# Kernel tuning notes

Measured on AMD Instinct MI355X. Metric: run time of the kernel, lower is better.

## Reference

```python
import jax, jax.numpy as jnp
import numpy as np

N_EMBD = 1024
N_HEAD = 16
HEAD_DIM = N_EMBD // N_HEAD


def setup_inputs() -> dict:
    key = jax.random.key(0)
    ks = jax.random.split(key, 5)
    B, T = 4, 2048
    s = 0.02
    return {
        "x": jax.random.normal(ks[0], (B, T, N_EMBD), dtype=jnp.float32),
        "w_qkv": jax.random.normal(ks[1], (N_EMBD, 3 * N_EMBD), dtype=jnp.float32) * s,
        "b_qkv": jnp.zeros((3 * N_EMBD,), dtype=jnp.float32),
        "w_out": jax.random.normal(ks[2], (N_EMBD, N_EMBD), dtype=jnp.float32) * s,
        "b_out": jnp.zeros((N_EMBD,), dtype=jnp.float32),
    }


def reference(x, w_qkv, b_qkv, w_out, b_out):
    # Eval-mode forward (dropout disabled), matching the torch module's math.
    B, T, C = x.shape
    qkv = x @ w_qkv + b_qkv                      # [B,T,3C]
    q, k, v = jnp.split(qkv, 3, axis=-1)
    def heads(t):
        return t.reshape(B, T, N_HEAD, HEAD_DIM).transpose(0, 2, 1, 3)  # [B,H,T,D]
    q, k, v = heads(q), heads(k), heads(v)
    scores = jnp.einsum("bhtd,bhsd->bhts", q, k) / jnp.sqrt(jnp.float32(HEAD_DIM))
    causal = jnp.tril(jnp.ones((T, T), dtype=bool))
    scores = jnp.where(causal[None, None], scores, -jnp.inf)
    attn = jax.nn.softmax(scores, axis=-1)       # [B,H,T,T]
    y = jnp.einsum("bhts,bhsd->bhtd", attn, v)   # [B,H,T,D]
    y = y.transpose(0, 2, 1, 3).reshape(B, T, C)
    return y @ w_out + b_out
```

## Files before the change

### kernel.cpp

```cpp
#include <hip/hip_runtime.h>
#include <hip/hip_bf16.h>

#define TSEQ 2048
#define CEMB 1024

typedef __attribute__((ext_vector_type(8))) short bf16x8;
typedef __attribute__((ext_vector_type(4))) float f32x4;
typedef __attribute__((ext_vector_type(16))) float f32x16;
typedef __attribute__((ext_vector_type(4))) int i32x4;

__device__ __forceinline__ unsigned short f2bf(float f){
  return __builtin_bit_cast(unsigned short, __float2bfloat16(f));
}

__device__ __forceinline__ f32x4 MFMA16(bf16x8 a, bf16x8 b, f32x4 c){
  return __builtin_amdgcn_mfma_f32_16x16x32_bf16(a, b, c, 0, 0, 0);
}

#define GLDS(src, dst) __builtin_amdgcn_global_load_lds( \
      (const __attribute__((address_space(1))) void*)(src), \
      (__attribute__((address_space(3))) void*)(dst), 16, 0, 0)

template<int N> __device__ __forceinline__ void vmwait(){
  if constexpr (N == 0) asm volatile("s_waitcnt vmcnt(0)" ::: "memory");
  else if constexpr (N == 6) asm volatile("s_waitcnt vmcnt(6)" ::: "memory");
  else if constexpr (N == 7) asm volatile("s_waitcnt vmcnt(7)" ::: "memory");
  else asm volatile("s_waitcnt vmcnt(8)" ::: "memory");
}

__global__ void k_cvt_bf16(const float* __restrict__ in, unsigned short* __restrict__ out, int n4){
  int i = blockIdx.x * blockDim.x + threadIdx.x;
  if (i >= n4) return;
  const float4 v = reinterpret_cast<const float4*>(in)[i];
  ushort4 o;
  o.x = f2bf(v.x); o.y = f2bf(v.y); o.z = f2bf(v.z); o.w = f2bf(v.w);
  reinterpret_cast<ushort4*>(out)[i] = o;
}

__global__ void k_transpose_bf16(const float* __restrict__ w, unsigned short* __restrict__ wT, int K, int N){
  __shared__ unsigned short tile[32][33];
  const int n0 = blockIdx.x * 32, k0 = blockIdx.y * 32;
  const int tx = threadIdx.x & 31, ty = threadIdx.x >> 5;
  #pragma unroll
  for (int r = 0; r < 4; ++r){
    int k = ty * 4 + r;
    tile[k][tx] = f2bf(w[(size_t)(k0 + k) * N + n0 + tx]);
  }
  __syncthreads();
  #pragma unroll
  for (int r = 0; r < 4; ++r){
    int n = ty * 4 + r;
    wT[(size_t)(n0 + n) * K + k0 + tx] = tile[tx][n];
  }
}

__global__ __launch_bounds__(256) void k_vT(const unsigned short* __restrict__ qkv,
                                            unsigned short* __restrict__ vT){
  __shared__ __align__(16) unsigned short tile[64*64];
  const int tid = threadIdx.x;
  const int bh = blockIdx.x;
  const int t0 = blockIdx.y * 64;
  const int b = bh >> 4, h = bh & 15;
  const int lt = tid >> 3, seg = tid & 7;
  #pragma unroll
  for (int r = 0; r < 2; ++r){
    const int t = lt + 32*r;
    const i32x4 v = *(const i32x4*)&qkv[((size_t)(b*TSEQ + t0 + t))*3072 + 2048 + h*64 + seg*8];
    const int slot = seg ^ (t & 7) ^ (t >> 3);
    *(i32x4*)((char*)tile + t*128 + slot*16) = v;
  }
  __syncthreads();
  const int w = tid >> 6, lane = tid & 63;
  const int tseg = lane & 7;
  #pragma unroll
  for (int r = 0; r < 2; ++r){
    const int d = w*8 + (lane>>3) + 32*r;
    unsigned int wd[4];
    #pragma unroll
    for (int jp = 0; jp < 4; ++jp){
      unsigned int lo, hi;
      #pragma unroll
      for (int e = 0; e < 2; ++e){
        const int j = jp*2 + e;
        const int t = tseg*8 + j;
        const int byteoff = t*128 + ((2*d) ^ (((j ^ tseg) & 7) << 4));
        const unsigned int val = *(const unsigned short*)((const char*)tile + byteoff);
        if (e == 0) lo = val; else hi = val;
      }
      wd[jp] = lo | (hi << 16);
    }
    i32x4 o4; o4[0]=wd[0]; o4[1]=wd[1]; o4[2]=wd[2]; o4[3]=wd[3];
    *(i32x4*)&vT[((size_t)bh*64 + d)*2048 + t0 + tseg*8] = o4;
  }
}

template<bool OUT_BF16, int BN>
__global__ __launch_bounds__(512, 2) void k_gemm256(
    const unsigned short* __restrict__ A,
    const unsigned short* __restrict__ Bt,
    const float* __restrict__ bias,
    void* __restrict__ Cout, int M, int N, int K)
{
  constexpr int NW  = BN / 64;
  constexpr int NH0 = (NW + 1) / 2;
  constexpr int NL  = 4 + NW;
  constexpr int BNB = BN * 128;
  __shared__ __align__(16) char smem[65536 + 2 * BNB];

  const int tid = threadIdx.x;
  const int lane = tid & 63, w = tid >> 6;
  const int wm = w >> 2, wn = w & 3;
  const int l15 = lane & 15, l4 = lane >> 4;
  const int x7 = l15 & 7;

  unsigned lin = blockIdx.x;
  {
    const unsigned nwg = gridDim.x;
    const unsigned qq = nwg >> 3, rr = nwg & 7;
    const unsigned xcd = lin & 7, loc = lin >> 3;
    lin = (xcd < rr ? xcd * (qq + 1) : rr * (qq + 1) + (xcd - rr) * qq) + loc;
  }
  const unsigned ntn = (unsigned)N / BN;
  const int m0 = (int)(lin / ntn) << 8;
  const int n0 = (int)(lin % ntn) * BN;

  const int srow = lane >> 3;
  const int scx  = (lane & 7) ^ srow;
  const unsigned short* Ag = A  + (size_t)(m0 + w*8 + srow) * K + scx * 8;
  const unsigned short* Bg = Bt + (size_t)(n0 + w*8 + srow) * K + scx * 8;

  auto stageA = [&](int buf, int kt){
    const unsigned short* s = Ag + kt*64;
    char* d = smem + buf*32768 + (w << 10);
    #pragma unroll
    for (int i = 0; i < 4; ++i) GLDS(s + (size_t)(i*64)*K, d + i*8192);
  };
  auto stageB = [&](int buf, int kt){
    const unsigned short* s = Bg + kt*64;
    char* d = smem + 65536 + buf*BNB + (w << 10);
    #pragma unroll
    for (int i = 0; i < NW; ++i) GLDS(s + (size_t)(i*64)*K, d + i*8192);
  };

  const int arow = wm*128 + l15;
  const int brow = wn*(BN/4) + l15;
  auto rdA = [&](int buf, int m, int ks)->bf16x8 {
    return *(const bf16x8*)(smem + buf*32768 + (arow + m*16)*128 + (((ks*4 + l4) ^ x7) << 4));
  };
  auto rdB = [&](int buf, int n, int ks)->bf16x8 {
    return *(const bf16x8*)(smem + 65536 + buf*BNB + (brow + n*16)*128 + (((ks*4 + l4) ^ x7) << 4));
  };

  f32x4 acc[8][NW] = {};
  const int NIT = K >> 7;

  stageA(0, 0); stageB(0, 0);
  stageA(1, 1); stageB(1, 1);
  vmwait<NL>();
  __builtin_amdgcn_s_barrier();
  asm volatile("" ::: "memory");

  for (int it = 0; it < NIT; ++it){
    const bool more = (it + 1 < NIT);
    #pragma unroll
    for (int half = 0; half < 2; ++half){
      const int buf = half;
      bf16x8 bfr[NW][2], af1[4][2], af2[4][2];
      #pragma unroll
      for (int n = 0; n < NW; ++n){ bfr[n][0] = rdB(buf, n, 0); bfr[n][1] = rdB(buf, n, 1); }
      #pragma unroll
      for (int m = 0; m < 4; ++m){ af1[m][0] = rdA(buf, m, 0); af1[m][1] = rdA(buf, m, 1); }
      __builtin_amdgcn_s_setprio(1);
      #pragma unroll
      for (int m = 0; m < 4; ++m)
        #pragma unroll
        for (int n = 0; n < NH0; ++n)
          #pragma unroll
          for (int ks = 0; ks < 2; ++ks)
            acc[m][n] = MFMA16(af1[m][ks], bfr[n][ks], acc[m][n]);
      __builtin_amdgcn_s_setprio(0);
      #pragma unroll
      for (int m = 0; m < 4; ++m){ af2[m][0] = rdA(buf, m+4, 0); af2[m][1] = rdA(buf, m+4, 1); }
      __builtin_amdgcn_s_setprio(1);
      #pragma unroll
      for (int m = 0; m < 4; ++m)
        #pragma unroll
        for (int n = NH0; n < NW; ++n)
          #pragma unroll
          for (int ks = 0; ks < 2; ++ks)
            acc[m][n] = MFMA16(af1[m][ks], bfr[n][ks], acc[m][n]);
      __builtin_amdgcn_s_setprio(0);
      __builtin_amdgcn_s_setprio(1);
      #pragma unroll
      for (int m = 0; m < 4; ++m)
        #pragma unroll
        for (int n = NH0; n < NW; ++n)
          #pragma unroll
          for (int ks = 0; ks < 2; ++ks)
            acc[m+4][n] = MFMA16(af2[m][ks], bfr[n][ks], acc[m+4][n]);
      __builtin_amdgcn_s_setprio(0);
      asm volatile("s_waitcnt lgkmcnt(0)" ::: "memory");
      __builtin_amdgcn_s_barrier();
      asm volatile("" ::: "memory");
      if (more){ stageA(buf, 2*it + half + 2); stageB(buf, 2*it + half + 2); }
      __builtin_amdgcn_s_setprio(1);
      #pragma unroll
      for (int m = 0; m < 4; ++m)
        #pragma unroll
        for (int n = 0; n < NH0; ++n)
          #pragma unroll
          for (int ks = 0; ks < 2; ++ks)
            acc[m+4][n] = MFMA16(af2[m][ks], bfr[n][ks], acc[m+4][n]);
      __builtin_amdgcn_s_setprio(0);
      if (more) vmwait<NL>();
      else      vmwait<0>();
      __builtin_amdgcn_s_barrier();
      asm volatile("" ::: "memory");
    }
  }

  float bv[NW];
  #pragma unroll
  for (int n = 0; n < NW; ++n) bv[n] = bias[n0 + wn*(BN/4) + n*16 + l15];

  #pragma unroll
  for (int m = 0; m < 8; ++m){
    const int row = m0 + wm*128 + m*16 + l4*4;
    #pragma unroll
    for (int n = 0; n < NW; ++n){
      const int col = n0 + wn*(BN/4) + n*16 + l15;
      #pragma unroll
      for (int r = 0; r < 4; ++r){
        float v = acc[m][n][r] + bv[n];
        if (OUT_BF16)
          ((unsigned short*)Cout)[(size_t)(row + r) * N + col] = f2bf(v);
        else
          ((float*)Cout)[(size_t)(row + r) * N + col] = v;
      }
    }
  }
}

__global__ __launch_bounds__(512, 4) void k_attn(
    const unsigned short* __restrict__ qkv,
    const unsigned short* __restrict__ vT,
    unsigned short* __restrict__ y)
{
  __shared__ __align__(16) char Ksm[2][8192];
  __shared__ __align__(16) char Vsm[2][8192];
  __shared__ float Ls[8][32];

  const int tid = threadIdx.x, lane = tid & 63, w = tid >> 6;
  const int q31 = lane & 31, hi = lane >> 5;
  const int bh = blockIdx.x, p = blockIdx.y;
  const int g = w >> 2, wl = w & 3;
  const int myt = g ? (15 - p) : p;
  const int b = bh >> 4, h = bh & 15;
  const size_t rowB = (size_t)b * TSEQ;

  const int wq0 = myt*128 + 32*wl, qg = wq0 + q31;
  const int nkt_my = 2*myt + 2;
  const int nktB  = 2*(15 - p) + 2;

  const float sc = 0.18033688011112042f;

  bf16x8 qf[4];
  {
    const unsigned short* qp = qkv + (rowB + qg) * 3072 + h * 64;
    #pragma unroll
    for (int c4 = 0; c4 < 4; ++c4){
      bf16x8 v = *(const bf16x8*)(qp + c4*16 + hi*8);
      #pragma unroll
      for (int j = 0; j < 8; ++j){
        const unsigned int bits = ((unsigned int)(unsigned short)v[j]) << 16;
        v[j] = (short)f2bf(__builtin_bit_cast(float, bits) * sc);
      }
      qf[c4] = v;
    }
  }

  const int kr = lane >> 3, sl = lane & 7, cx = sl ^ kr;
  const unsigned short* kgbase = qkv + (rowB + w*8 + kr) * 3072 + 1024 + h*64 + cx*8;
  const unsigned short* vgbase = vT + ((size_t)bh*64 + w*8 + kr) * 2048 + cx*8;

  #define STAGE(ktile, buf)                                                          \
    do {                                                                             \
      GLDS(kgbase + (size_t)(ktile)*64*3072, &Ksm[buf][0] + w*1024);                 \
      GLDS(vgbase + (ktile)*64,              &Vsm[buf][0] + w*1024);                 \
    } while (0)

  f32x16 O[2] = {};
  float l = 0.f;

  STAGE(0, 0);
  __syncthreads();

  int cbuf = 0;
  for (int kt = 0; kt < nktB; ++kt){
    if (kt + 1 < nktB) STAGE(kt + 1, cbuf ^ 1);

    if (kt < nkt_my){
      const char* kb = Ksm[cbuf];
      const char* vb = Vsm[cbuf];
      const bool domask = (kt*64 + 63 > wq0);
      #pragma unroll
      for (int sub = 0; sub < 2; ++sub){
        f32x16 S = {};
        __builtin_amdgcn_s_setprio(1);
        #pragma unroll
        for (int c4 = 0; c4 < 4; ++c4){
          const bf16x8 kf = *(const bf16x8*)(kb + (sub*32 + q31)*128
                                + ((((c4<<1)|hi) ^ (q31 & 7)) << 4));
          S = __builtin_amdgcn_mfma_f32_32x32x16_bf16(kf, qf[c4], S, 0, 0, 0);
        }
        __builtin_amdgcn_s_setprio(0);
        if (domask){
          #pragma unroll
          for (int r = 0; r < 16; ++r){
            const int kg = kt*64 + sub*32 + (r&3) + 8*(r>>2) + 4*hi;
            if (kg > qg) S[r] = -1e30f;
          }
        }
        float ps = 0.f;
        #pragma unroll
        for (int r = 0; r < 16; ++r){
          S[r] = __builtin_amdgcn_exp2f(S[r]);
          ps += S[r];
        }
        l += ps;
        bf16x8 paf[2];
        #pragma unroll
        for (int kc = 0; kc < 2; ++kc){
          const int e = kc * 8;
          unsigned int a, bb, cc, dd;
          asm("v_cvt_pk_bf16_f32 %0, %1, %2" : "=v"(a)  : "v"(S[e+0]), "v"(S[e+1]));
          asm("v_cvt_pk_bf16_f32 %0, %1, %2" : "=v"(bb) : "v"(S[e+4]), "v"(S[e+5]));
          asm("v_cvt_pk_bf16_f32 %0, %1, %2" : "=v"(cc) : "v"(S[e+2]), "v"(S[e+3]));
          asm("v_cvt_pk_bf16_f32 %0, %1, %2" : "=v"(dd) : "v"(S[e+6]), "v"(S[e+7]));
          asm volatile("v_permlane32_swap_b32 %0, %1" : "+v"(a),  "+v"(bb));
          asm volatile("v_permlane32_swap_b32 %0, %1" : "+v"(cc), "+v"(dd));
          i32x4 pwv; pwv[0] = (int)a; pwv[1] = (int)cc; pwv[2] = (int)bb; pwv[3] = (int)dd;
          paf[kc] = __builtin_bit_cast(bf16x8, pwv);
        }
        __builtin_amdgcn_s_setprio(1);
        #pragma unroll
        for (int kc = 0; kc < 2; ++kc){
          #pragma unroll
          for (int dblk = 0; dblk < 2; ++dblk){
            const int dr = dblk*32 + q31;
            const bf16x8 vf = *(const bf16x8*)(vb + dr*128
                                  + ((((sub<<2)|(kc<<1)|hi) ^ (dr & 7)) << 4));
            O[dblk] = __builtin_amdgcn_mfma_f32_32x32x16_bf16(paf[kc], vf, O[dblk], 0, 0, 0);
          }
        }
        __builtin_amdgcn_s_setprio(0);
      }
    }

    __syncthreads();
    cbuf ^= 1;
  }

  {
    const float lc = l + __shfl_xor(l, 32);
    if (lane < 32) Ls[w][lane] = 1.0f / lc;
  }
  __syncthreads();

  #pragma unroll
  for (int r = 0; r < 16; ++r){
    const int qloc = (r&3) + 8*(r>>2) + 4*hi;
    const float inv = Ls[w][qloc];
    const size_t row = rowB + wq0 + qloc;
    #pragma unroll
    for (int dblk = 0; dblk < 2; ++dblk)
      y[row * CEMB + h*64 + dblk*32 + q31] = f2bf(O[dblk][r] * inv);
  }
  #undef STAGE
}

extern "C" void kernel_launch(void* const* d_in, const int* in_sizes, int n_in,
                              void* d_out, int out_size, void* d_ws, size_t ws_size,
                              hipStream_t stream)
{
  const float* x     = (const float*)d_in[0];
  const float* w_qkv = (const float*)d_in[1];
  const float* b_qkv = (const float*)d_in[2];
  const float* w_out = (const float*)d_in[3];
  const float* b_out = (const float*)d_in[4];
  float* out = (float*)d_out;

  char* ws = (char*)d_ws;
  unsigned short* xb    = (unsigned short*)(ws);
  unsigned short* vTb   = (unsigned short*)(ws);
  unsigned short* qkvb  = (unsigned short*)(ws + (16u<<20));
  unsigned short* yb    = (unsigned short*)(ws + (64u<<20));
  unsigned short* wqkvT = (unsigned short*)(ws + (80u<<20));
  unsigned short* woutT = (unsigned short*)(ws + (86u<<20));

  const int M = 4 * TSEQ;

  k_cvt_bf16<<<(M * CEMB / 4 + 255) / 256, 256, 0, stream>>>(x, xb, M * CEMB / 4);
  k_transpose_bf16<<<dim3(3072/32, 1024/32), 256, 0, stream>>>(w_qkv, wqkvT, 1024, 3072);
  k_transpose_bf16<<<dim3(1024/32, 1024/32), 256, 0, stream>>>(w_out, woutT, 1024, 1024);

  k_gemm256<true, 192><<<dim3((M/256) * (3072/192)), 512, 0, stream>>>(xb, wqkvT, b_qkv, qkvb, M, 3072, 1024);
  k_vT<<<dim3(64, TSEQ/64), 256, 0, stream>>>(qkvb, vTb);
  k_attn<<<dim3(4 * 16, 8), 512, 0, stream>>>(qkvb, vTb, yb);
  k_gemm256<false, 128><<<dim3((M/256) * (1024/128)), 512, 0, stream>>>(yb, woutT, b_out, out, M, 1024, 1024);
}
```

Before: 159.2 us.

## Fuse prep kernels, reorder attention grid, relax attention launch bounds

Merges the input bf16 conversion and both weight transpose kernels into a single launch that dispatches work by block index, removing two kernel launches. The attention grid is swapped so the query-tile index is the fast dimension, which changes the order in which heads and tiles are scheduled across CUs. The attention kernel's minimum blocks-per-CU hint drops from 4 to 3, giving the compiler more registers at the cost of possible lower occupancy.

```diff
diff --git a/kernel.cpp b/kernel.cpp
--- a/kernel.cpp
+++ b/kernel.cpp
@@ -28,19 +28,32 @@
   else asm volatile("s_waitcnt vmcnt(8)" ::: "memory");
 }
 
-__global__ void k_cvt_bf16(const float* __restrict__ in, unsigned short* __restrict__ out, int n4){
-  int i = blockIdx.x * blockDim.x + threadIdx.x;
-  if (i >= n4) return;
-  const float4 v = reinterpret_cast<const float4*>(in)[i];
-  ushort4 o;
-  o.x = f2bf(v.x); o.y = f2bf(v.y); o.z = f2bf(v.z); o.w = f2bf(v.w);
-  reinterpret_cast<ushort4*>(out)[i] = o;
-}
-
-__global__ void k_transpose_bf16(const float* __restrict__ w, unsigned short* __restrict__ wT, int K, int N){
+__global__ __launch_bounds__(256) void k_prep(
+    const float* __restrict__ x, unsigned short* __restrict__ xb,
+    const float* __restrict__ w_qkv, unsigned short* __restrict__ wqkvT,
+    const float* __restrict__ w_out, unsigned short* __restrict__ woutT)
+{
   __shared__ unsigned short tile[32][33];
-  const int n0 = blockIdx.x * 32, k0 = blockIdx.y * 32;
-  const int tx = threadIdx.x & 31, ty = threadIdx.x >> 5;
+  const int bid = blockIdx.x, tid = threadIdx.x;
+  if (bid < 8192){
+    const int i = bid * 256 + tid;
+    const float4 v = reinterpret_cast<const float4*>(x)[i];
+    ushort4 o;
+    o.x = f2bf(v.x); o.y = f2bf(v.y); o.z = f2bf(v.z); o.w = f2bf(v.w);
+    reinterpret_cast<ushort4*>(xb)[i] = o;
+    return;
+  }
+  const float* w; unsigned short* wT; int N, n0, k0;
+  if (bid < 11264){
+    const int b2 = bid - 8192;
+    w = w_qkv; wT = wqkvT; N = 3072;
+    n0 = (b2 % 96) * 32; k0 = (b2 / 96) * 32;
+  } else {
+    const int b3 = bid - 11264;
+    w = w_out; wT = woutT; N = 1024;
+    n0 = (b3 & 31) * 32; k0 = (b3 >> 5) * 32;
+  }
+  const int tx = tid & 31, ty = tid >> 5;
   #pragma unroll
   for (int r = 0; r < 4; ++r){
     int k = ty * 4 + r;
@@ -50,7 +63,7 @@
   #pragma unroll
   for (int r = 0; r < 4; ++r){
     int n = ty * 4 + r;
-    wT[(size_t)(n0 + n) * K + k0 + tx] = tile[tx][n];
+    wT[(size_t)(n0 + n) * 1024 + k0 + tx] = tile[tx][n];
   }
 }
 
@@ -241,7 +254,7 @@
   }
 }
 
-__global__ __launch_bounds__(512, 4) void k_attn(
+__global__ __launch_bounds__(512, 3) void k_attn(
     const unsigned short* __restrict__ qkv,
     const unsigned short* __restrict__ vT,
     unsigned short* __restrict__ y)
@@ -252,7 +265,7 @@
 
   const int tid = threadIdx.x, lane = tid & 63, w = tid >> 6;
   const int q31 = lane & 31, hi = lane >> 5;
-  const int bh = blockIdx.x, p = blockIdx.y;
+  const int p = blockIdx.x, bh = blockIdx.y;
   const int g = w >> 2, wl = w & 3;
   const int myt = g ? (15 - p) : p;
   const int b = bh >> 4, h = bh & 15;
@@ -279,7 +292,7 @@
     }
   }
 
-  const int kr = lane >> 3, sl = lane & 7, cx = sl ^ kr;
+  const int kr = lane >> 3, cx = (lane & 7) ^ kr;
   const unsigned short* kgbase = qkv + (rowB + w*8 + kr) * 3072 + 1024 + h*64 + cx*8;
   const unsigned short* vgbase = vT + ((size_t)bh*64 + w*8 + kr) * 2048 + cx*8;
 
@@ -400,12 +413,10 @@
 
   const int M = 4 * TSEQ;
 
-  k_cvt_bf16<<<(M * CEMB / 4 + 255) / 256, 256, 0, stream>>>(x, xb, M * CEMB / 4);
-  k_transpose_bf16<<<dim3(3072/32, 1024/32), 256, 0, stream>>>(w_qkv, wqkvT, 1024, 3072);
-  k_transpose_bf16<<<dim3(1024/32, 1024/32), 256, 0, stream>>>(w_out, woutT, 1024, 1024);
+  k_prep<<<12288, 256, 0, stream>>>(x, xb, w_qkv, wqkvT, w_out, woutT);
 
   k_gemm256<true, 192><<<dim3((M/256) * (3072/192)), 512, 0, stream>>>(xb, wqkvT, b_qkv, qkvb, M, 3072, 1024);
   k_vT<<<dim3(64, TSEQ/64), 256, 0, stream>>>(qkvb, vTb);
-  k_attn<<<dim3(4 * 16, 8), 512, 0, stream>>>(qkvb, vTb, yb);
+  k_attn<<<dim3(8, 4 * 16), 512, 0, stream>>>(qkvb, vTb, yb);
   k_gemm256<false, 128><<<dim3((M/256) * (1024/128)), 512, 0, stream>>>(yb, woutT, b_out, out, M, 1024, 1024);
 }
```

Result: no change. 161.6 us (+1.5%).
